# Kernel optimization log

Measured on AMD Instinct MI355X. Metric: run time of the kernel, lower is better.

## Reference

```python
import jax, jax.numpy as jnp
import numpy as np

IMG = 512
B = 4
NA = 3          # anchors per location
NC = 3          # classes
K = 512         # pre-NMS top-k per image per level (<= smallest level anchor count 768)
STRIDES = [4, 8, 16, 32]
MIN_S = [0.01, 0.02, 0.03, 0.04]
MAX_S = [0.06, 0.08, 0.10, 0.12]
W_SC = [0.8, 0.9, 1.0, 1.1]
H_SC = [1.0, 1.2, 1.4, 1.6]
CONF_T = 0.15
NMS_T = 0.5
STD = 0.2       # box_delta_stds (means are 0)


def make_anchors(stride):
    H = IMG // stride
    c = (np.arange(H) + 0.5) * stride
    cy, cx = np.meshgrid(c, c, indexing='ij')           # [H, W]
    sizes = stride * 4.0 * (2.0 ** (np.arange(NA) / 3.0))  # [A]
    cx = np.broadcast_to(cx, (NA, H, H))
    cy = np.broadcast_to(cy, (NA, H, H))
    s = sizes[:, None, None]
    # A-major, then H, W -- matches permute(0,1,3,4,2).reshape flattening
    anc = np.stack([cx - s / 2, cy - s / 2, cx + s / 2, cy + s / 2], -1).reshape(-1, 4)
    return jnp.asarray(anc, jnp.float32)


def setup_inputs() -> dict:
    key = jax.random.key(0)
    ks = jax.random.split(key, 8)
    inp = {}
    for l, s in enumerate(STRIDES):
        H = IMG // s
        inp[f'cls{l}'] = jax.random.normal(ks[2 * l], (B, NA, NC, H, H), jnp.float32)
        inp[f'box{l}'] = jax.random.normal(ks[2 * l + 1], (B, NA, 4, H, H), jnp.float32)
        inp[f'anc{l}'] = make_anchors(s)
    inp['image_size'] = IMG
    return inp


def decode_level(cls, box, anc, lvl, image_size):
    Bc, A, C, H, W = cls.shape
    scores = jax.nn.sigmoid(jnp.transpose(cls, (0, 1, 3, 4, 2)).reshape(Bc, -1, C))  # [B,N,C]
    d = jnp.transpose(box, (0, 1, 3, 4, 2)).reshape(Bc, -1, 4)                        # [B,N,4]
    img = jnp.asarray(image_size, jnp.float32)
    aw = (anc[:, 2] - anc[:, 0]) / img
    ah = (anc[:, 3] - anc[:, 1]) / img
    acx = (anc[:, 0] + anc[:, 2]) * 0.5 / img
    acy = (anc[:, 1] + anc[:, 3]) * 0.5 / img
    fs = 1.0 / STRIDES[lvl]
    dx = jnp.clip(d[..., 0] * STD, -1.0, 1.0) * fs * aw
    dy = jnp.clip(d[..., 1] * STD, -1.0, 1.0) * fs * ah
    cx = jnp.clip(acx + dx, 0.0, 1.0)
    cy = jnp.clip(acy + dy, 0.0, 1.0)
    dw = jnp.clip(d[..., 2] * STD, -2.0, 2.0)
    dh = jnp.clip(d[..., 3] * STD, -2.0, 2.0)
    pw = jnp.clip(aw * W_SC[lvl] * jnp.exp(dw * (0.2 + 0.1 * lvl)), MIN_S[lvl] * 0.8, MAX_S[lvl] * 0.9)
    ph = jnp.clip(ah * H_SC[lvl] * jnp.exp(dh * (0.4 + 0.2 * lvl)), MIN_S[lvl] * 0.8, MAX_S[lvl] * 1.2)
    boxes = jnp.stack([
        jnp.clip(cx - 0.5 * pw, 0.0, 1.0),
        jnp.clip(cy - 0.5 * ph, 0.0, 1.0),
        jnp.clip(cx + 0.5 * pw, 0.0, 1.0),
        jnp.clip(cy + 0.5 * ph, 0.0, 1.0)], -1)                                       # [B,N,4]
    ms = scores.max(-1)
    mc = scores.argmax(-1)
    w = boxes[..., 2] - boxes[..., 0]
    h = boxes[..., 3] - boxes[..., 1]
    valid = (ms > CONF_T) & (w > MIN_S[lvl] * 0.5) & (h > MIN_S[lvl] * 0.5) \
            & (w < MAX_S[lvl] * 2.0) & (h < MAX_S[lvl] * 2.0)
    # pre-NMS top-k on (masked) scores
    sort_key = jnp.where(valid, ms, -1.0)
    _, idx = jax.lax.top_k(sort_key, K)                                               # [B,K]
    boxes_k = jnp.take_along_axis(boxes, idx[..., None], 1)
    scores_k = jnp.take_along_axis(ms, idx, 1)
    labels_k = jnp.take_along_axis(mc, idx, 1)
    valid_k = jnp.take_along_axis(valid, idx, 1)
    return boxes_k, scores_k, labels_k, valid_k


def pairwise_iou(b):
    area = (b[:, 2] - b[:, 0]) * (b[:, 3] - b[:, 1])
    lt = jnp.maximum(b[:, None, :2], b[None, :, :2])
    rb = jnp.minimum(b[:, None, 2:], b[None, :, 2:])
    wh = jnp.clip(rb - lt, 0.0)
    inter = wh[..., 0] * wh[..., 1]
    return inter / (area[:, None] + area[None, :] - inter + 1e-9)


def nms_keep(boxes, valid):
    # boxes sorted by descending score; sequential greedy NMS
    iou = pairwise_iou(boxes)                 # [K,K]
    rank = jnp.arange(K)
    def body(i, keep):
        overlap = jnp.max(jnp.where((rank < i) & keep, iou[i], 0.0))
        return keep.at[i].set(valid[i] & (overlap <= NMS_T))
    return jax.lax.fori_loop(0, K, body, jnp.zeros((K,), bool))


def reference(cls0, box0, anc0, cls1, box1, anc1, cls2, box2, anc2, cls3, box3, anc3, image_size):
    levels = [(cls0, box0, anc0), (cls1, box1, anc1), (cls2, box2, anc2), (cls3, box3, anc3)]
    outs = [decode_level(c, b, a, l, image_size) for l, (c, b, a) in enumerate(levels)]
    boxes = jnp.stack([o[0] for o in outs], 1)    # [B, L, K, 4]
    scores = jnp.stack([o[1] for o in outs], 1)   # [B, L, K]
    labels = jnp.stack([o[2] for o in outs], 1)   # [B, L, K]
    valid = jnp.stack([o[3] for o in outs], 1)    # [B, L, K]
    keep = jax.vmap(jax.vmap(nms_keep))(boxes, valid)
    boxes = jnp.where(keep[..., None], boxes, 0.0)
    scores = jnp.where(keep, scores, 0.0)
    labels = jnp.where(keep, labels + 1, 0)       # torch code returns labels + 1
    return boxes, scores, labels, keep
```

## Files before the change

### kernel.cpp

```cpp
#include <hip/hip_runtime.h>
#include <math.h>

#define K_TOP 512
#define CAND_CAP 3072

struct LvlC {
  int H, lgH, HH, lgHH;
  float fs, wsc, hsc, wex, hex, pwlo, pwhi, phlo, phhi, minwh, maxwh;
};

__device__ const LvlC LVL[4] = {
  {128, 7, 16384, 14, 0.25f,    0.8f, 1.0f, 0.2f, 0.4f, 0.008f, 0.054f, 0.008f, 0.072f, 0.005f, 0.12f},
  { 64, 6,  4096, 12, 0.125f,   0.9f, 1.2f, 0.3f, 0.6f, 0.016f, 0.072f, 0.016f, 0.096f, 0.01f,  0.16f},
  { 32, 5,  1024, 10, 0.0625f,  1.0f, 1.4f, 0.4f, 0.8f, 0.024f, 0.09f,  0.024f, 0.12f,  0.015f, 0.2f },
  { 16, 4,   256,  8, 0.03125f, 1.1f, 1.6f, 0.5f, 1.0f, 0.032f, 0.108f, 0.032f, 0.144f, 0.02f,  0.24f},
};

__device__ const float TSEL[4] = {0.91f, 0.85f, 0.65f, -2.0f};

__device__ __forceinline__ void decode_box(const LvlC& L, const float* __restrict__ boxp,
                                           const float* __restrict__ ancp,
                                           int b, int idx, float rimg,
                                           float& x0, float& y0, float& x1, float& y1)
{
#pragma clang fp contract(off)
  int a   = idx >> L.lgHH;
  int rem = idx & (L.HH - 1);
  const float* bp = boxp + (size_t)((b * 3 + a) * 4) * L.HH + rem;
  float d0 = bp[0], d1 = bp[L.HH], d2 = bp[2 * L.HH], d3 = bp[3 * L.HH];
  float4 av = reinterpret_cast<const float4*>(ancp)[idx];
  float a0 = av.x, a1 = av.y, a2 = av.z, a3 = av.w;
  float aw  = (a2 - a0) * rimg;
  float ah  = (a3 - a1) * rimg;
  float acx = (a0 + a2) * 0.5f * rimg;
  float acy = (a1 + a3) * 0.5f * rimg;
  float dx = fminf(fmaxf(d0 * 0.2f, -1.f), 1.f) * L.fs * aw;
  float dy = fminf(fmaxf(d1 * 0.2f, -1.f), 1.f) * L.fs * ah;
  float cx = fminf(fmaxf(acx + dx, 0.f), 1.f);
  float cy = fminf(fmaxf(acy + dy, 0.f), 1.f);
  float dw = fminf(fmaxf(d2 * 0.2f, -2.f), 2.f);
  float dh = fminf(fmaxf(d3 * 0.2f, -2.f), 2.f);
  float pw = fminf(fmaxf(aw * L.wsc * expf(dw * L.wex), L.pwlo), L.pwhi);
  float ph = fminf(fmaxf(ah * L.hsc * expf(dh * L.hex), L.phlo), L.phhi);
  x0 = fminf(fmaxf(cx - 0.5f * pw, 0.f), 1.f);
  y0 = fminf(fmaxf(cy - 0.5f * ph, 0.f), 1.f);
  x1 = fminf(fmaxf(cx + 0.5f * pw, 0.f), 1.f);
  y1 = fminf(fmaxf(cy + 0.5f * ph, 0.f), 1.f);
}

__device__ __forceinline__ void seg_map(int blk, int& b, int& l, int& base, int& iblk)
{
  b = blk / 255;
  int rb = blk - b * 255;
  if (rb < 192)      { l = 0; iblk = rb;       base = 0;     }
  else if (rb < 240) { l = 1; iblk = rb - 192; base = 49152; }
  else if (rb < 252) { l = 2; iblk = rb - 240; base = 61440; }
  else               { l = 3; iblk = rb - 252; base = 64512; }
}

__global__ __launch_bounds__(256) void dc_kernel(
    const float* __restrict__ cls0, const float* __restrict__ box0, const float* __restrict__ anc0,
    const float* __restrict__ cls1, const float* __restrict__ box1, const float* __restrict__ anc1,
    const float* __restrict__ cls2, const float* __restrict__ box2, const float* __restrict__ anc2,
    const float* __restrict__ cls3, const float* __restrict__ box3, const float* __restrict__ anc3,
    const int* __restrict__ imgp, unsigned long long* __restrict__ keys,
    unsigned long long* __restrict__ cand, unsigned* __restrict__ unitCnt)
{
  __shared__ unsigned wcnt[4];
  int unit = (int)blockIdx.x;
  int tid = (int)threadIdx.x;
  int wid = tid >> 6, lane = tid & 63;
  int b, l, base, iblk;
  seg_map(unit, b, l, base, iblk);
  int i = iblk * 256 + tid;

  const float *cls, *boxp, *ancp;
  switch (l) {
    case 0:  cls = cls0; boxp = box0; ancp = anc0; break;
    case 1:  cls = cls1; boxp = box1; ancp = anc1; break;
    case 2:  cls = cls2; boxp = box2; ancp = anc2; break;
    default: cls = cls3; boxp = box3; ancp = anc3; break;
  }
  LvlC L = LVL[l];
  float rimg = 1.0f / (float)(*imgp);

  int a   = i >> L.lgHH;
  int rem = i & (L.HH - 1);
  const float* cp = cls + (size_t)((b * 3 + a) * 3) * L.HH + rem;
  float c0 = cp[0], c1 = cp[L.HH], c2 = cp[2 * L.HH];
  float m = c0; int mc = 0;
  if (c1 > m) { m = c1; mc = 1; }
  if (c2 > m) { m = c2; mc = 2; }
  float ms = 1.f / (1.f + expf(-m));

  float x0, y0, x1, y1;
  decode_box(L, boxp, ancp, b, i, rimg, x0, y0, x1, y1);
  float w = x1 - x0, h = y1 - y0;
  bool valid = (ms > 0.15f) && (w > L.minwh) && (h > L.minwh) && (w < L.maxwh) && (h < L.maxwh);

  float sk = valid ? ms : -1.0f;
  unsigned u = __float_as_uint(sk);
  unsigned ascu  = (u & 0x80000000u) ? ~u : (u | 0x80000000u);
  unsigned descu = ~ascu;
  unsigned long long key = ((unsigned long long)descu << 32)
                         | ((unsigned long long)(unsigned)i << 16)
                         | ((unsigned)mc << 8) | (valid ? 1u : 0u);
  keys[(size_t)b * 65280 + base + i] = key;

  bool take = (sk >= TSEL[l]);
  unsigned long long bm = __ballot(take);
  if (lane == 0) wcnt[wid] = (unsigned)__popcll(bm);
  __syncthreads();
  if (take) {
    unsigned off = 0;
    for (int w2 = 0; w2 < wid; ++w2) off += wcnt[w2];
    off += (unsigned)__popcll(bm & ((1ull << lane) - 1ull));
    cand[(size_t)unit * 256 + off] = key;
  }
  if (tid == 0) unitCnt[unit] = wcnt[0] + wcnt[1] + wcnt[2] + wcnt[3];
}

__global__ __launch_bounds__(512) void sel_kernel(
    const unsigned long long* __restrict__ keys,
    const unsigned long long* __restrict__ cand, const unsigned* __restrict__ unitCnt,
    const float* __restrict__ box0, const float* __restrict__ anc0,
    const float* __restrict__ box1, const float* __restrict__ anc1,
    const float* __restrict__ box2, const float* __restrict__ anc2,
    const float* __restrict__ box3, const float* __restrict__ anc3,
    const int* __restrict__ imgp,
    float* __restrict__ boxesWS, float* __restrict__ scoresWS,
    int* __restrict__ labelsWS, unsigned* __restrict__ validWS)
{
  __shared__ unsigned long long scand[CAND_CAP];
  __shared__ unsigned long long skey[K_TOP];
  __shared__ unsigned long long skey2[K_TOP];
  __shared__ unsigned hist[8][256];
  __shared__ unsigned upref[256];
  __shared__ unsigned ucnt_s[256];
  __shared__ unsigned waveSum[8];
  __shared__ unsigned long long shPrefix;
  __shared__ unsigned shBelow, shCnt, shTotal;

  int seg = (int)blockIdx.x;
  int b = seg >> 2, l = seg & 3;
  int tid = (int)threadIdx.x;
  const int nt = 512;
  int wid = tid >> 6, lane = tid & 63;

  const int nArr[4]    = {49152, 12288, 3072, 768};
  const int baseArr[4] = {0, 49152, 61440, 64512};
  const int nuArr[4]   = {192, 48, 12, 3};
  const int fuArr[4]   = {0, 192, 240, 252};
  int N = nArr[l];
  int nu = nuArr[l];
  int firstU = b * 255 + fuArr[l];
  const unsigned long long* kp = keys + (size_t)b * 65280 + baseArr[l];

  if (tid == 0) { shPrefix = 0ull; shBelow = 0u; shCnt = 0u; }

  unsigned c = (tid < nu) ? unitCnt[firstU + tid] : 0u;
  if (tid < 256) ucnt_s[tid] = c;
  unsigned incl = c;
  for (int off = 1; off < 64; off <<= 1) {
    unsigned n = __shfl_up(incl, off);
    if (lane >= off) incl += n;
  }
  if (lane == 63) waveSum[wid] = incl;
  __syncthreads();
  if (tid < 256) {
    unsigned add = 0;
    for (int w2 = 0; w2 < wid; ++w2) add += waveSum[w2];
    if (tid < nu) upref[tid] = incl - c + add;
  }
  if (tid == 0) shTotal = waveSum[0] + waveSum[1] + waveSum[2] + waveSum[3];
  __syncthreads();

  unsigned total = shTotal;
  bool useCand = (total >= K_TOP && total <= CAND_CAP);
  int M = useCand ? (int)total : N;

  if (useCand) {
    for (int f = tid; f < (int)total; f += nt) {
      int lo = 0, hi = nu - 1;
      while (lo < hi) {
        int mid = (lo + hi + 1) >> 1;
        if ((int)upref[mid] <= f) lo = mid; else hi = mid - 1;
      }
      scand[f] = cand[(size_t)(firstU + lo) * 256 + (unsigned)(f - (int)upref[lo])];
    }
  }
  __syncthreads();

  for (int r = 0; r < 6; ++r) {
    int shift = 56 - 8 * r;
    for (int v = tid; v < 8 * 256; v += nt) ((unsigned*)hist)[v] = 0u;
    __syncthreads();
    unsigned long long pref = shPrefix;
    unsigned below = shBelow;
    unsigned long long hiMask = (r == 0) ? 0ull : (~0ull << (64 - 8 * r));
    for (int t = tid; t < M; t += nt) {
      unsigned long long k = useCand ? scand[t] : kp[t];
      if ((k & hiMask) == (pref & hiMask))
        atomicAdd(&hist[wid][(unsigned)((k >> shift) & 0xFF)], 1u);
    }
    __syncthreads();
    unsigned s = 0, incl2 = 0;
    if (tid < 256) {
#pragma unroll
      for (int w2 = 0; w2 < 8; ++w2) s += hist[w2][tid];
      incl2 = s;
    }
    for (int off = 1; off < 64; off <<= 1) {
      unsigned n = __shfl_up(incl2, off);
      if (lane >= off) incl2 += n;
    }
    if (lane == 63) waveSum[wid] = incl2;
    __syncthreads();
    if (tid < 256) {
      unsigned add = 0;
      for (int w2 = 0; w2 < wid; ++w2) add += waveSum[w2];
      unsigned inclT = incl2 + add;
      unsigned exclT = inclT - s;
      if (below + exclT < K_TOP && below + inclT >= K_TOP) {
        shBelow = below + exclT;
        shPrefix = pref | ((unsigned long long)(unsigned)tid << shift);
      }
    }
    __syncthreads();
  }
  unsigned long long kth = shPrefix | 0xFFFFull;

  for (int t = tid; t < M; t += nt) {
    unsigned long long k = useCand ? scand[t] : kp[t];
    bool take = (k <= kth);
    unsigned long long bm = __ballot(take);
    unsigned bp = 0;
    if (lane == 0 && bm) bp = atomicAdd(&shCnt, (unsigned)__popcll(bm));
    bp = __shfl(bp, 0);
    if (take) skey[bp + (unsigned)__popcll(bm & ((1ull << lane) - 1ull))] = k;
  }
  __syncthreads();

  {
    unsigned long long mykey = skey[tid];
    int rank = 0;
#pragma unroll 8
    for (int j = 0; j < K_TOP; ++j) rank += (skey[j] < mykey) ? 1 : 0;
    skey2[rank] = mykey;
  }
  __syncthreads();

  const float *boxp, *ancp;
  switch (l) {
    case 0:  boxp = box0; ancp = anc0; break;
    case 1:  boxp = box1; ancp = anc1; break;
    case 2:  boxp = box2; ancp = anc2; break;
    default: boxp = box3; ancp = anc3; break;
  }
  LvlC L = LVL[l];
  float rimg = 1.0f / (float)(*imgp);
  {
    unsigned long long key = skey2[tid];
    int idx = (int)((key >> 16) & 0xFFFFull);
    unsigned descu = (unsigned)(key >> 32);
    unsigned ascu  = ~descu;
    unsigned u = (ascu & 0x80000000u) ? (ascu & 0x7FFFFFFFu) : ~ascu;
    float x0, y0, x1, y1;
    decode_box(L, boxp, ancp, b, idx, rimg, x0, y0, x1, y1);
    int o = seg * K_TOP + tid;
    float4 bb; bb.x = x0; bb.y = y0; bb.z = x1; bb.w = y1;
    reinterpret_cast<float4*>(boxesWS)[o] = bb;
    scoresWS[o] = __uint_as_float(u);
    labelsWS[o] = (int)((key >> 8) & 0xFFull);
    validWS[o]  = (unsigned)(key & 1ull);
  }
}

__global__ __launch_bounds__(256) void mask_kernel(
    const float* __restrict__ boxesWS, unsigned long long* __restrict__ masks)
{
#pragma clang fp contract(off)
  int blk = (int)blockIdx.x;
  int seg = blk >> 5;
  int wid = (int)threadIdx.x >> 6;
  int lane = (int)threadIdx.x & 63;
  int waveInSeg = (blk & 31) * 4 + wid;
  const float4* bb = reinterpret_cast<const float4*>(boxesWS) + seg * K_TOP;
  unsigned long long* mseg = masks + (size_t)seg * K_TOP * 8;

  float4 bj[8]; float aj[8];
#pragma unroll
  for (int c = 0; c < 8; ++c) {
    bj[c] = bb[c * 64 + lane];
    aj[c] = (bj[c].z - bj[c].x) * (bj[c].w - bj[c].y);
  }
#pragma unroll
  for (int rr = 0; rr < 4; ++rr) {
    int r = waveInSeg * 4 + rr;
    float4 br = bb[r];
    float ar_ = (br.z - br.x) * (br.w - br.y);
#pragma unroll
    for (int c = 0; c < 8; ++c) {
      float ltx = fmaxf(br.x, bj[c].x), lty = fmaxf(br.y, bj[c].y);
      float rbx = fminf(br.z, bj[c].z), rby = fminf(br.w, bj[c].w);
      float ww = fmaxf(rbx - ltx, 0.f), hh = fmaxf(rby - lty, 0.f);
      float inter = ww * hh;
      float iou = inter / (ar_ + aj[c] - inter + 1e-9f);
      unsigned long long bal = __ballot(iou > 0.5f);
      if (lane == 0) mseg[c * K_TOP + r] = bal;
    }
  }
}

__global__ __launch_bounds__(512) void scan_kernel(
    const unsigned long long* __restrict__ masks,
    const float* __restrict__ boxesWS, const float* __restrict__ scoresWS,
    const int* __restrict__ labelsWS, const unsigned* __restrict__ validWS,
    float* __restrict__ out)
{
  __shared__ unsigned long long sMaskT[8 * K_TOP];
  __shared__ unsigned long long keepWords[8];
  __shared__ unsigned sChanged;

  int seg = (int)blockIdx.x;
  int tid = (int)threadIdx.x;
  int wid = tid >> 6, lane = tid & 63;
  const unsigned long long* mp = masks + (size_t)seg * K_TOP * 8;
#pragma unroll
  for (int w = 0; w < 8; ++w) sMaskT[w * K_TOP + tid] = mp[w * K_TOP + tid];
  bool valid = validWS[seg * K_TOP + tid] != 0u;

  unsigned long long myWord = __ballot(valid);
  if (lane == 0) keepWords[wid] = myWord;
  __syncthreads();

  for (int it = 0; it < 513; ++it) {
    unsigned long long sup = 0ull;
    for (int w = 0; w < wid; ++w)
      sup |= sMaskT[w * K_TOP + tid] & keepWords[w];
    sup |= sMaskT[wid * K_TOP + tid] & keepWords[wid] & ((1ull << lane) - 1ull);
    bool nk = valid && (sup == 0ull);
    unsigned long long nw = __ballot(nk);
    __syncthreads();
    if (tid == 0) sChanged = 0u;
    __syncthreads();
    if (lane == 0) {
      if (nw != keepWords[wid]) sChanged = 1u;
      keepWords[wid] = nw;
    }
    __syncthreads();
    if (sChanged == 0u) break;
  }

  int o = seg * K_TOP + tid;
  bool keep = (keepWords[wid] >> lane) & 1ull;
  float4 bx = reinterpret_cast<const float4*>(boxesWS)[o];
  float4 ob;
  ob.x = keep ? bx.x : 0.f;
  ob.y = keep ? bx.y : 0.f;
  ob.z = keep ? bx.z : 0.f;
  ob.w = keep ? bx.w : 0.f;
  reinterpret_cast<float4*>(out)[o] = ob;
  out[32768 + o] = keep ? scoresWS[o] : 0.f;
  out[40960 + o] = keep ? (float)(labelsWS[o] + 1) : 0.f;
  out[49152 + o] = keep ? 1.f : 0.f;
}

extern "C" void kernel_launch(void* const* d_in, const int* in_sizes, int n_in,
                              void* d_out, int out_size, void* d_ws, size_t ws_size,
                              hipStream_t stream)
{
  const float* cls0 = (const float*)d_in[0];
  const float* box0 = (const float*)d_in[1];
  const float* anc0 = (const float*)d_in[2];
  const float* cls1 = (const float*)d_in[3];
  const float* box1 = (const float*)d_in[4];
  const float* anc1 = (const float*)d_in[5];
  const float* cls2 = (const float*)d_in[6];
  const float* box2 = (const float*)d_in[7];
  const float* anc2 = (const float*)d_in[8];
  const float* cls3 = (const float*)d_in[9];
  const float* box3 = (const float*)d_in[10];
  const float* anc3 = (const float*)d_in[11];
  const int*   imgp = (const int*)d_in[12];

  char* ws = (char*)d_ws;
  unsigned long long* keys    = (unsigned long long*)(ws + 0);
  unsigned long long* cand    = (unsigned long long*)(ws + 2088960);
  unsigned*           unitCnt = (unsigned*)(ws + 4177920);
  float*              boxesWS = (float*)(ws + 4182016);
  float*              scoresWS= (float*)(ws + 4313088);
  int*                labelsWS= (int*)(ws + 4345856);
  unsigned*           validWS = (unsigned*)(ws + 4378624);
  unsigned long long* masks   = (unsigned long long*)(ws + 4411392);
  float* out = (float*)d_out;

  dc_kernel<<<1020, 256, 0, stream>>>(cls0, box0, anc0, cls1, box1, anc1,
                                      cls2, box2, anc2, cls3, box3, anc3,
                                      imgp, keys, cand, unitCnt);
  sel_kernel<<<16, 512, 0, stream>>>(keys, cand, unitCnt,
                                     box0, anc0, box1, anc1, box2, anc2, box3, anc3,
                                     imgp, boxesWS, scoresWS, labelsWS, validWS);
  mask_kernel<<<512, 256, 0, stream>>>(boxesWS, masks);
  scan_kernel<<<16, 512, 0, stream>>>(masks, boxesWS, scoresWS, labelsWS, validWS, out);
}
```

Measured before the change: 117.2 us.

## Fuse selection, IoU mask, and NMS scan into one per-segment kernel

The selection, IoU mask and NMS scan kernels become a single post_kernel with one block per (image, level) segment. Boxes, scores and labels stay in registers and shared memory instead of round-tripping through workspace, and the IoU mask matrix is built directly in shared memory that aliases the selection buffers. This removes two launches and the global writes and reads of intermediates. In exchange, the mask computation that used 512 blocks now runs on only 16 blocks, each wave looping over 64 rows, so parallelism drops sharply for that phase.

```diff
diff --git a/kernel.cpp b/kernel.cpp
--- a/kernel.cpp
+++ b/kernel.cpp
@@ -120,26 +120,28 @@
   if (tid == 0) unitCnt[unit] = wcnt[0] + wcnt[1] + wcnt[2] + wcnt[3];
 }
 
-__global__ __launch_bounds__(512) void sel_kernel(
+__global__ __launch_bounds__(512) void post_kernel(
     const unsigned long long* __restrict__ keys,
     const unsigned long long* __restrict__ cand, const unsigned* __restrict__ unitCnt,
     const float* __restrict__ box0, const float* __restrict__ anc0,
     const float* __restrict__ box1, const float* __restrict__ anc1,
     const float* __restrict__ box2, const float* __restrict__ anc2,
     const float* __restrict__ box3, const float* __restrict__ anc3,
-    const int* __restrict__ imgp,
-    float* __restrict__ boxesWS, float* __restrict__ scoresWS,
-    int* __restrict__ labelsWS, unsigned* __restrict__ validWS)
-{
-  __shared__ unsigned long long scand[CAND_CAP];
-  __shared__ unsigned long long skey[K_TOP];
-  __shared__ unsigned long long skey2[K_TOP];
-  __shared__ unsigned hist[8][256];
+    const int* __restrict__ imgp, float* __restrict__ out)
+{
+#pragma clang fp contract(off)
+  __shared__ alignas(16) char smem[40960];
+  unsigned long long* scand  = (unsigned long long*)(smem);
+  unsigned long long* skey   = (unsigned long long*)(smem + 24576);
+  unsigned long long* skey2  = (unsigned long long*)(smem + 28672);
+  unsigned (*hist)[256]      = (unsigned (*)[256])(smem + 32768);
+  float4* sbox               = (float4*)(smem);
+  unsigned long long* smaskT = (unsigned long long*)(smem + 8192);
   __shared__ unsigned upref[256];
-  __shared__ unsigned ucnt_s[256];
   __shared__ unsigned waveSum[8];
+  __shared__ unsigned long long keepWords[8];
   __shared__ unsigned long long shPrefix;
-  __shared__ unsigned shBelow, shCnt, shTotal;
+  __shared__ unsigned shBelow, shCnt, shTotal, sChanged;
 
   int seg = (int)blockIdx.x;
   int b = seg >> 2, l = seg & 3;
@@ -159,7 +161,6 @@
   if (tid == 0) { shPrefix = 0ull; shBelow = 0u; shCnt = 0u; }
 
   unsigned c = (tid < nu) ? unitCnt[firstU + tid] : 0u;
-  if (tid < 256) ucnt_s[tid] = c;
   unsigned incl = c;
   for (int off = 1; off < 64; off <<= 1) {
     unsigned n = __shfl_up(incl, off);
@@ -259,76 +260,43 @@
   }
   LvlC L = LVL[l];
   float rimg = 1.0f / (float)(*imgp);
+
+  unsigned long long key = skey2[tid];
+  int idx = (int)((key >> 16) & 0xFFFFull);
+  unsigned descu = (unsigned)(key >> 32);
+  unsigned ascu  = ~descu;
+  unsigned u = (ascu & 0x80000000u) ? (ascu & 0x7FFFFFFFu) : ~ascu;
+  int label = (int)((key >> 8) & 0xFFull);
+  bool valid = (key & 1ull) != 0ull;
+  float x0, y0, x1, y1;
+  decode_box(L, boxp, ancp, b, idx, rimg, x0, y0, x1, y1);
+  __syncthreads();
+  float4 mybox; mybox.x = x0; mybox.y = y0; mybox.z = x1; mybox.w = y1;
+  sbox[tid] = mybox;
+  __syncthreads();
+
   {
-    unsigned long long key = skey2[tid];
-    int idx = (int)((key >> 16) & 0xFFFFull);
-    unsigned descu = (unsigned)(key >> 32);
-    unsigned ascu  = ~descu;
-    unsigned u = (ascu & 0x80000000u) ? (ascu & 0x7FFFFFFFu) : ~ascu;
-    float x0, y0, x1, y1;
-    decode_box(L, boxp, ancp, b, idx, rimg, x0, y0, x1, y1);
-    int o = seg * K_TOP + tid;
-    float4 bb; bb.x = x0; bb.y = y0; bb.z = x1; bb.w = y1;
-    reinterpret_cast<float4*>(boxesWS)[o] = bb;
-    scoresWS[o] = __uint_as_float(u);
-    labelsWS[o] = (int)((key >> 8) & 0xFFull);
-    validWS[o]  = (unsigned)(key & 1ull);
-  }
-}
-
-__global__ __launch_bounds__(256) void mask_kernel(
-    const float* __restrict__ boxesWS, unsigned long long* __restrict__ masks)
-{
-#pragma clang fp contract(off)
-  int blk = (int)blockIdx.x;
-  int seg = blk >> 5;
-  int wid = (int)threadIdx.x >> 6;
-  int lane = (int)threadIdx.x & 63;
-  int waveInSeg = (blk & 31) * 4 + wid;
-  const float4* bb = reinterpret_cast<const float4*>(boxesWS) + seg * K_TOP;
-  unsigned long long* mseg = masks + (size_t)seg * K_TOP * 8;
-
-  float4 bj[8]; float aj[8];
+    float4 bj[8]; float aj[8];
 #pragma unroll
-  for (int c = 0; c < 8; ++c) {
-    bj[c] = bb[c * 64 + lane];
-    aj[c] = (bj[c].z - bj[c].x) * (bj[c].w - bj[c].y);
-  }
+    for (int cc = 0; cc < 8; ++cc) {
+      bj[cc] = sbox[cc * 64 + lane];
+      aj[cc] = (bj[cc].z - bj[cc].x) * (bj[cc].w - bj[cc].y);
+    }
+    for (int r = wid * 64; r < wid * 64 + 64; ++r) {
+      float4 br = sbox[r];
+      float ar_ = (br.z - br.x) * (br.w - br.y);
 #pragma unroll
-  for (int rr = 0; rr < 4; ++rr) {
-    int r = waveInSeg * 4 + rr;
-    float4 br = bb[r];
-    float ar_ = (br.z - br.x) * (br.w - br.y);
-#pragma unroll
-    for (int c = 0; c < 8; ++c) {
-      float ltx = fmaxf(br.x, bj[c].x), lty = fmaxf(br.y, bj[c].y);
-      float rbx = fminf(br.z, bj[c].z), rby = fminf(br.w, bj[c].w);
-      float ww = fmaxf(rbx - ltx, 0.f), hh = fmaxf(rby - lty, 0.f);
-      float inter = ww * hh;
-      float iou = inter / (ar_ + aj[c] - inter + 1e-9f);
-      unsigned long long bal = __ballot(iou > 0.5f);
-      if (lane == 0) mseg[c * K_TOP + r] = bal;
-    }
-  }
-}
-
-__global__ __launch_bounds__(512) void scan_kernel(
-    const unsigned long long* __restrict__ masks,
-    const float* __restrict__ boxesWS, const float* __restrict__ scoresWS,
-    const int* __restrict__ labelsWS, const unsigned* __restrict__ validWS,
-    float* __restrict__ out)
-{
-  __shared__ unsigned long long sMaskT[8 * K_TOP];
-  __shared__ unsigned long long keepWords[8];
-  __shared__ unsigned sChanged;
-
-  int seg = (int)blockIdx.x;
-  int tid = (int)threadIdx.x;
-  int wid = tid >> 6, lane = tid & 63;
-  const unsigned long long* mp = masks + (size_t)seg * K_TOP * 8;
-#pragma unroll
-  for (int w = 0; w < 8; ++w) sMaskT[w * K_TOP + tid] = mp[w * K_TOP + tid];
-  bool valid = validWS[seg * K_TOP + tid] != 0u;
+      for (int cc = 0; cc < 8; ++cc) {
+        float ltx = fmaxf(br.x, bj[cc].x), lty = fmaxf(br.y, bj[cc].y);
+        float rbx = fminf(br.z, bj[cc].z), rby = fminf(br.w, bj[cc].w);
+        float ww = fmaxf(rbx - ltx, 0.f), hh = fmaxf(rby - lty, 0.f);
+        float inter = ww * hh;
+        float iou = inter / (ar_ + aj[cc] - inter + 1e-9f);
+        unsigned long long bal = __ballot(iou > 0.5f);
+        if (lane == 0) smaskT[cc * K_TOP + r] = bal;
+      }
+    }
+  }
 
   unsigned long long myWord = __ballot(valid);
   if (lane == 0) keepWords[wid] = myWord;
@@ -337,8 +305,8 @@
   for (int it = 0; it < 513; ++it) {
     unsigned long long sup = 0ull;
     for (int w = 0; w < wid; ++w)
-      sup |= sMaskT[w * K_TOP + tid] & keepWords[w];
-    sup |= sMaskT[wid * K_TOP + tid] & keepWords[wid] & ((1ull << lane) - 1ull);
+      sup |= smaskT[w * K_TOP + tid] & keepWords[w];
+    sup |= smaskT[wid * K_TOP + tid] & keepWords[wid] & ((1ull << lane) - 1ull);
     bool nk = valid && (sup == 0ull);
     unsigned long long nw = __ballot(nk);
     __syncthreads();
@@ -354,15 +322,14 @@
 
   int o = seg * K_TOP + tid;
   bool keep = (keepWords[wid] >> lane) & 1ull;
-  float4 bx = reinterpret_cast<const float4*>(boxesWS)[o];
   float4 ob;
-  ob.x = keep ? bx.x : 0.f;
-  ob.y = keep ? bx.y : 0.f;
-  ob.z = keep ? bx.z : 0.f;
-  ob.w = keep ? bx.w : 0.f;
+  ob.x = keep ? mybox.x : 0.f;
+  ob.y = keep ? mybox.y : 0.f;
+  ob.z = keep ? mybox.z : 0.f;
+  ob.w = keep ? mybox.w : 0.f;
   reinterpret_cast<float4*>(out)[o] = ob;
-  out[32768 + o] = keep ? scoresWS[o] : 0.f;
-  out[40960 + o] = keep ? (float)(labelsWS[o] + 1) : 0.f;
+  out[32768 + o] = keep ? __uint_as_float(u) : 0.f;
+  out[40960 + o] = keep ? (float)(label + 1) : 0.f;
   out[49152 + o] = keep ? 1.f : 0.f;
 }
 
@@ -388,19 +355,12 @@
   unsigned long long* keys    = (unsigned long long*)(ws + 0);
   unsigned long long* cand    = (unsigned long long*)(ws + 2088960);
   unsigned*           unitCnt = (unsigned*)(ws + 4177920);
-  float*              boxesWS = (float*)(ws + 4182016);
-  float*              scoresWS= (float*)(ws + 4313088);
-  int*                labelsWS= (int*)(ws + 4345856);
-  unsigned*           validWS = (unsigned*)(ws + 4378624);
-  unsigned long long* masks   = (unsigned long long*)(ws + 4411392);
   float* out = (float*)d_out;
 
   dc_kernel<<<1020, 256, 0, stream>>>(cls0, box0, anc0, cls1, box1, anc1,
                                       cls2, box2, anc2, cls3, box3, anc3,
                                       imgp, keys, cand, unitCnt);
-  sel_kernel<<<16, 512, 0, stream>>>(keys, cand, unitCnt,
-                                     box0, anc0, box1, anc1, box2, anc2, box3, anc3,
-                                     imgp, boxesWS, scoresWS, labelsWS, validWS);
-  mask_kernel<<<512, 256, 0, stream>>>(boxesWS, masks);
-  scan_kernel<<<16, 512, 0, stream>>>(masks, boxesWS, scoresWS, labelsWS, validWS, out);
-}
+  post_kernel<<<16, 512, 0, stream>>>(keys, cand, unitCnt,
+                                      box0, anc0, box1, anc1, box2, anc2, box3, anc3,
+                                      imgp, out);
+}
```

Result: slower. 156.5 us (+33.5%).
